# Performance work log

Hardware: AMD Instinct MI355X
Metric: run time of the kernel (lower is better)

## Reference

```python
import jax, jax.numpy as jnp
import numpy as np

N_HEADS = 32
N_KV_HEADS = 8


def _rope_tables(T, half_dim):
    # standard rotary angle tables: theta_i = 10000^(-2i/D)
    inv_freq = 1.0 / (10000.0 ** (np.arange(half_dim, dtype=np.float32) / half_dim))
    ang = np.arange(T, dtype=np.float32)[:, None] * inv_freq[None, :]  # [T, D/2]
    return jnp.asarray(np.sin(ang)), jnp.asarray(np.cos(ang))


def setup_inputs() -> dict:
    key = jax.random.key(0)
    ks = jax.random.split(key, 5)
    B, T, C = 1, 2048, 2048
    hd = C // N_HEADS  # 64
    kv_dim = N_KV_HEADS * hd  # 512
    w_scale = 0.02
    x = jax.random.normal(ks[0], (B, T, C), dtype=jnp.float32)
    Wq = jax.random.normal(ks[1], (C, C), dtype=jnp.float32) * w_scale
    Wk = jax.random.normal(ks[2], (C, kv_dim), dtype=jnp.float32) * w_scale
    Wv = jax.random.normal(ks[3], (C, kv_dim), dtype=jnp.float32) * w_scale
    Wo = jax.random.normal(ks[4], (C, C), dtype=jnp.float32) * w_scale
    rope_sin, rope_cos = _rope_tables(T, hd // 2)
    return {"x": x, "Wq": Wq, "Wk": Wk, "Wv": Wv, "Wo": Wo,
            "rope_sin": rope_sin, "rope_cos": rope_cos, "swa_window": 1024}


def apply_rope(x, sin, cos):
    # x: [B, T, H, D]; sin/cos: [T, D/2]; interleaved-pair rotation
    B, T, H, D = x.shape
    xr = x.reshape(B, T, H, D // 2, 2)
    x1, x2 = xr[..., 0], xr[..., 1]
    s = sin[None, :, None, :]
    c = cos[None, :, None, :]
    o1 = x1 * c - x2 * s
    o2 = x1 * s + x2 * c
    return jnp.stack((o1, o2), axis=-1).reshape(B, T, H, D)


def reference(x, Wq, Wk, Wv, Wo, rope_sin, rope_cos, swa_window):
    B, T, C = x.shape
    hd = C // N_HEADS
    g = N_HEADS // N_KV_HEADS
    q = (x @ Wq).reshape(B, T, N_HEADS, hd)
    k = (x @ Wk).reshape(B, T, N_KV_HEADS, hd)
    v = (x @ Wv).reshape(B, T, N_KV_HEADS, hd)
    q = apply_rope(q, rope_sin, rope_cos)
    k = apply_rope(k, rope_sin, rope_cos)
    # GQA: expand kv heads (repeat_interleave along head dim)
    k = jnp.repeat(k, g, axis=2)
    v = jnp.repeat(v, g, axis=2)
    q = q.transpose(0, 2, 1, 3)  # [B, H, T, D]
    k = k.transpose(0, 2, 1, 3)
    v = v.transpose(0, 2, 1, 3)
    scores = jnp.einsum('bhqd,bhkd->bhqk', q, k) / jnp.sqrt(jnp.float32(hd))
    idx = jnp.arange(T)
    rel = idx[:, None] - idx[None, :]  # query_pos - key_pos
    # masked-out: future tokens (rel < 0) or older than the sliding window
    masked = (rel < 0) | (rel > swa_window)
    scores = jnp.where(masked[None, None], jnp.float32(-1e30), scores)
    attn = jax.nn.softmax(scores, axis=-1)
    out = jnp.einsum('bhqk,bhkd->bhqd', attn, v)
    out = out.transpose(0, 2, 1, 3).reshape(B, T, C)
    return out @ Wo
```

## Files before the change

### kernel.cpp

```cpp
#include <hip/hip_runtime.h>

typedef __attribute__((ext_vector_type(8))) short short8;
typedef __attribute__((ext_vector_type(4))) float f32x4;
typedef unsigned short u16;

#define T_SEQ 2048
#define C_DIM 2048
#define QKV_N 3072
#define HD 64
#define QSCALE 0.18033688011112042f


static __device__ __forceinline__ u16 f2bf(float f) {
    unsigned u = __builtin_bit_cast(unsigned, f);
    unsigned rounding = 0x7fffu + ((u >> 16) & 1u);
    return (u16)((u + rounding) >> 16);
}

static __device__ __forceinline__ void gld_lds16(void* lds, const void* g) {
    __builtin_amdgcn_global_load_lds(
        (const __attribute__((address_space(1))) unsigned int*)g,
        (__attribute__((address_space(3))) unsigned int*)lds, 16, 0, 0);
}


__global__ __launch_bounds__(256) void prep_all(const float* __restrict__ x,
                                                const float* __restrict__ Wq,
                                                const float* __restrict__ Wk,
                                                const float* __restrict__ Wv,
                                                const float* __restrict__ Wo,
                                                u16* __restrict__ xb,
                                                u16* __restrict__ Wt,
                                                u16* __restrict__ Wot) {
    __shared__ float tile[32][33];
    int bx = blockIdx.x;
    if (bx >= 160) {
        int id = (bx - 160) * 64 + blockIdx.y;
        int i = (id * 256 + threadIdx.x) * 4;
        f32x4 v = *(const f32x4*)(x + i);
        u16* o = xb + i;
        o[0] = f2bf(v[0]); o[1] = f2bf(v[1]); o[2] = f2bf(v[2]); o[3] = f2bf(v[3]);
        return;
    }
    const float* W; u16* D; int N, row_off;
    if (bx < 64)      { W = Wq; D = Wt;  N = 2048; row_off = 0;    }
    else if (bx < 80) { W = Wk; D = Wt;  N = 512;  row_off = 2048; bx -= 64; }
    else if (bx < 96) { W = Wv; D = Wt;  N = 512;  row_off = 2560; bx -= 80; }
    else              { W = Wo; D = Wot; N = 2048; row_off = 0;    bx -= 96; }
    int n0 = bx * 32, k0 = blockIdx.y * 32;
    int tx = threadIdx.x & 31, ty = threadIdx.x >> 5;
#pragma unroll
    for (int i = 0; i < 4; i++)
        tile[ty + i * 8][tx] = W[(size_t)(k0 + ty + i * 8) * N + n0 + tx];
    __syncthreads();
#pragma unroll
    for (int i = 0; i < 4; i++)
        D[(size_t)(row_off + n0 + ty + i * 8) * 2048 + k0 + tx] = f2bf(tile[tx][ty + i * 8]);
}


__global__ __launch_bounds__(256) void gemm_qkv(const u16* __restrict__ A,
                                                const u16* __restrict__ BT,
                                                const float* __restrict__ sn,
                                                const float* __restrict__ cs,
                                                u16* __restrict__ qb,
                                                u16* __restrict__ kb,
                                                u16* __restrict__ vb) {
    const int K = 2048;
    __shared__ alignas(16) u16 As[2][128][64];
    __shared__ alignas(16) u16 Bs[2][96][64];
    const int m0 = blockIdx.x * 128;
    const int bn0 = blockIdx.y * 96;
    const int w = threadIdx.x >> 6, lane = threadIdx.x & 63;
    const int lo = lane & 15, hi = lane >> 4;
    const int wr = w >> 1, wc = w & 1;
    const int srcsw = ((lane & 7) ^ (lane >> 3)) * 8;

    f32x4 zero4 = {0.f, 0.f, 0.f, 0.f};
    f32x4 acc[4][3];
#pragma unroll
    for (int m = 0; m < 4; m++)
#pragma unroll
        for (int n = 0; n < 3; n++) acc[m][n] = zero4;

    auto stage = [&](int buf, int k0) {
#pragma unroll
        for (int j = 0; j < 7; j++) {
            int s = j * 4 + w;
            if (s < 16) {
                int row = s * 8 + (lane >> 3);
                gld_lds16((char*)&As[buf][0][0] + s * 1024,
                          A + (size_t)(m0 + row) * K + k0 + srcsw);
            } else {
                int s2 = s - 16;
                int row = s2 * 8 + (lane >> 3);
                gld_lds16((char*)&Bs[buf][0][0] + s2 * 1024,
                          BT + (size_t)(bn0 + row) * K + k0 + srcsw);
            }
        }
    };

    stage(0, 0);
    __syncthreads();
    const int nk = K >> 6;
    for (int t = 0; t < nk; t++) {
        const int cur = t & 1;
        if (t + 1 < nk) stage(cur ^ 1, (t + 1) * 64);
#pragma unroll
        for (int kk = 0; kk < 2; kk++) {
            const int csw = ((kk * 4 + hi) ^ (lo & 7)) << 4;
            short8 a[4], b[3];
#pragma unroll
            for (int m = 0; m < 4; m++) {
                int r = wr * 64 + m * 16 + lo;
                a[m] = *(const short8*)((const char*)&As[cur][0][0] + r * 128 + csw);
            }
#pragma unroll
            for (int n = 0; n < 3; n++) {
                int r = wc * 48 + n * 16 + lo;
                b[n] = *(const short8*)((const char*)&Bs[cur][0][0] + r * 128 + csw);
            }
#pragma unroll
            for (int m = 0; m < 4; m++)
#pragma unroll
                for (int n = 0; n < 3; n++)
                    acc[m][n] = __builtin_amdgcn_mfma_f32_16x16x32_bf16(a[m], b[n], acc[m][n], 0, 0, 0);
        }
        __syncthreads();
    }
    const bool odd = (lo & 1);
#pragma unroll
    for (int m = 0; m < 4; m++)
#pragma unroll
        for (int n = 0; n < 3; n++) {
            const int col = bn0 + wc * 48 + n * 16 + lo;
#pragma unroll
            for (int r = 0; r < 4; r++) {
                const int trow = m0 + wr * 64 + m * 16 + hi * 4 + r;
                float v = acc[m][n][r];
                float p = __shfl_xor(v, 1);
                if (col >= 2560) {
                    vb[(size_t)trow * 512 + (col - 2560)] = f2bf(v);
                } else {
                    const int pr = (col & 63) >> 1;
                    const float s = sn[trow * 32 + pr], c = cs[trow * 32 + pr];
                    float o = odd ? (p * s + v * c) : (v * c - p * s);
                    if (col < 2048) {
                        qb[(size_t)trow * C_DIM + col] = f2bf(o * QSCALE);
                    } else {
                        const int cc = col - 2048;
                        kb[((size_t)(cc >> 6) * T_SEQ + trow) * 64 + (cc & 63)] = f2bf(o);
                    }
                }
            }
        }
}


template <int NF>
__global__ __launch_bounds__(256) void gemm_bt(const u16* __restrict__ A,
                                               const u16* __restrict__ BT,
                                               float* __restrict__ C,
                                               int M, int N, int K) {
    __shared__ alignas(16) u16 As[2][128][64];
    __shared__ alignas(16) u16 Bs[2][32 * NF][64];
    const int m0 = blockIdx.x * 128;
    const int bn0 = blockIdx.y * (32 * NF);
    const int w = threadIdx.x >> 6, lane = threadIdx.x & 63;
    const int lo = lane & 15, hi = lane >> 4;
    const int wr = w >> 1, wc = w & 1;
    const int srcsw = ((lane & 7) ^ (lane >> 3)) * 8;

    f32x4 zero4 = {0.f, 0.f, 0.f, 0.f};
    f32x4 acc[4][NF];
#pragma unroll
    for (int m = 0; m < 4; m++)
#pragma unroll
        for (int n = 0; n < NF; n++) acc[m][n] = zero4;

    const int NSEG = 16 + 4 * NF;
    auto stage = [&](int buf, int k0) {
#pragma unroll
        for (int j = 0; j < NSEG / 4; j++) {
            int s = j * 4 + w;
            if (s < 16) {
                int row = s * 8 + (lane >> 3);
                gld_lds16((char*)&As[buf][0][0] + s * 1024,
                          A + (size_t)(m0 + row) * K + k0 + srcsw);
            } else {
                int s2 = s - 16;
                int row = s2 * 8 + (lane >> 3);
                gld_lds16((char*)&Bs[buf][0][0] + s2 * 1024,
                          BT + (size_t)(bn0 + row) * K + k0 + srcsw);
            }
        }
    };

    stage(0, 0);
    __syncthreads();
    const int nk = K >> 6;
    for (int t = 0; t < nk; t++) {
        const int cur = t & 1;
        if (t + 1 < nk) stage(cur ^ 1, (t + 1) * 64);
#pragma unroll
        for (int kk = 0; kk < 2; kk++) {
            const int csw = ((kk * 4 + hi) ^ (lo & 7)) << 4;
            short8 a[4], b[NF];
#pragma unroll
            for (int m = 0; m < 4; m++) {
                int r = wr * 64 + m * 16 + lo;
                a[m] = *(const short8*)((const char*)&As[cur][0][0] + r * 128 + csw);
            }
#pragma unroll
            for (int n = 0; n < NF; n++) {
                int r = wc * 16 * NF + n * 16 + lo;
                b[n] = *(const short8*)((const char*)&Bs[cur][0][0] + r * 128 + csw);
            }
#pragma unroll
            for (int m = 0; m < 4; m++)
#pragma unroll
                for (int n = 0; n < NF; n++)
                    acc[m][n] = __builtin_amdgcn_mfma_f32_16x16x32_bf16(a[m], b[n], acc[m][n], 0, 0, 0);
        }
        __syncthreads();
    }
#pragma unroll
    for (int m = 0; m < 4; m++)
#pragma unroll
        for (int n = 0; n < NF; n++) {
            int col = bn0 + wc * 16 * NF + n * 16 + lo;
#pragma unroll
            for (int r = 0; r < 4; r++) {
                int row = m0 + wr * 64 + m * 16 + hi * 4 + r;
                C[(size_t)row * N + col] = acc[m][n][r];
            }
        }
}


__global__ __launch_bounds__(256) void vtrans(const u16* __restrict__ vb,
                                              u16* __restrict__ vt) {
    __shared__ unsigned tile[64][65];
    const int kvh = blockIdx.x >> 5, t0 = (blockIdx.x & 31) * 64;
    const int tx = threadIdx.x & 63, ty = threadIdx.x >> 6;
#pragma unroll
    for (int i = 0; i < 16; i++) {
        int r = ty * 16 + i;
        tile[r][tx] = vb[(size_t)(t0 + r) * 512 + kvh * 64 + tx];
    }
    __syncthreads();
#pragma unroll
    for (int i = 0; i < 16; i++) {
        int d = ty * 16 + i;
        vt[((size_t)kvh * 64 + d) * T_SEQ + t0 + tx] = (u16)tile[tx][d];
    }
}


__global__ __launch_bounds__(256) void attn_fwd(const u16* __restrict__ qb,
                                                const u16* __restrict__ kb,
                                                const u16* __restrict__ vt,
                                                u16* __restrict__ ob,
                                                const int* __restrict__ winp) {
    __shared__ alignas(16) char KsB[2][8192];
    __shared__ alignas(16) char VsB[2][8192];
    __shared__ alignas(16) u16 Ps[4][16][64];
    const int window = *winp;
    const int h = blockIdx.y, kvh = h >> 2;
    const int q0 = blockIdx.x * 64;
    const int w = threadIdx.x >> 6, lane = threadIdx.x & 63;
    const int lo = lane & 15, hi = lane >> 4;

    const int qrow = q0 + w * 16 + lo;
    const short8 qa0 = *(const short8*)(qb + (size_t)qrow * C_DIM + h * HD + hi * 8);
    const short8 qa1 = *(const short8*)(qb + (size_t)qrow * C_DIM + h * HD + 32 + hi * 8);

    f32x4 zero4 = {0.f, 0.f, 0.f, 0.f};
    f32x4 acc[4];
#pragma unroll
    for (int dt = 0; dt < 4; dt++) acc[dt] = zero4;
    float lreg[4] = {0.f, 0.f, 0.f, 0.f};

    int kt0 = q0 - window; if (kt0 < 0) kt0 = 0; kt0 &= ~63;
    const int qlo_w = q0 + w * 16, qhi_w = qlo_w + 15;
    const int nt = (q0 + 64 - kt0) >> 6;

    auto stage = [&](int buf, int kt) {
#pragma unroll
        for (int j = 0; j < 2; j++) {
            int c = (w * 2 + j) * 64 + lane;
            int rr = c >> 3, sc = (c & 7) ^ (rr & 7);
            gld_lds16(KsB[buf] + (w * 2 + j) * 1024,
                      kb + ((size_t)kvh * T_SEQ + kt + rr) * 64 + sc * 8);
            gld_lds16(VsB[buf] + (w * 2 + j) * 1024,
                      vt + ((size_t)kvh * 64 + rr) * T_SEQ + kt + sc * 8);
        }
    };

    stage(0, kt0);
    __syncthreads();
    for (int i = 0; i < nt; i++) {
        const int kt = kt0 + i * 64;
        const int cur = i & 1;
        if (i + 1 < nt) stage(cur ^ 1, kt + 64);
        if (kt <= qhi_w && kt + 63 >= qlo_w - window) {
            const bool interior = (kt + 63 <= qlo_w) && (qhi_w - kt <= window);
            f32x4 s0, s1, s2, s3;
            __builtin_amdgcn_s_setprio(1);
            {
#define QK_TILE(SD, NT)                                                              \
                {                                                                    \
                    int key = (NT) * 16 + lo;                                        \
                    const short8 kf0 = *(const short8*)(KsB[cur] + key * 128 + ((hi ^ (key & 7)) << 4));       \
                    const short8 kf1 = *(const short8*)(KsB[cur] + key * 128 + (((4 + hi) ^ (key & 7)) << 4)); \
                    f32x4 z = zero4;                                                 \
                    z = __builtin_amdgcn_mfma_f32_16x16x32_bf16(qa0, kf0, z, 0, 0, 0);\
                    z = __builtin_amdgcn_mfma_f32_16x16x32_bf16(qa1, kf1, z, 0, 0, 0);\
                    SD = z;                                                          \
                }
                QK_TILE(s0, 0) QK_TILE(s1, 1) QK_TILE(s2, 2) QK_TILE(s3, 3)
#undef QK_TILE
            }
            __builtin_amdgcn_s_setprio(0);
            if (!interior) {
#define MASK_TILE(SD, NT)                                                            \
                {                                                                    \
                    int key = kt + (NT) * 16 + lo;                                   \
                    _Pragma("unroll")                                                \
                    for (int r = 0; r < 4; r++) {                                    \
                        int q = qlo_w + hi * 4 + r;                                  \
                        if ((unsigned)(q - key) > (unsigned)window) SD[r] = -1e30f;  \
                    }                                                                \
                }
                MASK_TILE(s0, 0) MASK_TILE(s1, 1) MASK_TILE(s2, 2) MASK_TILE(s3, 3)
#undef MASK_TILE
            }
#define EXP_TILE(SD, NT)                                                             \
            {                                                                        \
                _Pragma("unroll")                                                    \
                for (int r = 0; r < 4; r++) {                                        \
                    float p = __builtin_amdgcn_exp2f(SD[r]);                         \
                    lreg[r] += p;                                                    \
                    int q16 = hi * 4 + r;                                            \
                    Ps[w][q16][((NT) * 16 + lo) ^ ((q16 & 7) << 3)] = f2bf(p);       \
                }                                                                    \
            }
            EXP_TILE(s0, 0) EXP_TILE(s1, 1) EXP_TILE(s2, 2) EXP_TILE(s3, 3)
#undef EXP_TILE
            const short8 pa0 = *(const short8*)&Ps[w][lo][(hi ^ (lo & 7)) << 3];
            const short8 pa1 = *(const short8*)&Ps[w][lo][((4 + hi) ^ (lo & 7)) << 3];
            __builtin_amdgcn_s_setprio(1);
#pragma unroll
            for (int dt = 0; dt < 4; dt++) {
                int d = dt * 16 + lo;
                const short8 vf0 = *(const short8*)(VsB[cur] + d * 128 + ((hi ^ (d & 7)) << 4));
                const short8 vf1 = *(const short8*)(VsB[cur] + d * 128 + (((4 + hi) ^ (d & 7)) << 4));
                acc[dt] = __builtin_amdgcn_mfma_f32_16x16x32_bf16(pa0, vf0, acc[dt], 0, 0, 0);
                acc[dt] = __builtin_amdgcn_mfma_f32_16x16x32_bf16(pa1, vf1, acc[dt], 0, 0, 0);
            }
            __builtin_amdgcn_s_setprio(0);
        }
        __syncthreads();
    }
    float inv[4];
#pragma unroll
    for (int r = 0; r < 4; r++) {
        float l = lreg[r];
        l += __shfl_xor(l, 1);
        l += __shfl_xor(l, 2);
        l += __shfl_xor(l, 4);
        l += __shfl_xor(l, 8);
        inv[r] = 1.0f / l;
    }
#pragma unroll
    for (int dt = 0; dt < 4; dt++)
#pragma unroll
        for (int r = 0; r < 4; r++) {
            int q = qlo_w + hi * 4 + r;
            ob[(size_t)q * C_DIM + h * HD + dt * 16 + lo] = f2bf(acc[dt][r] * inv[r]);
        }
}


extern "C" void kernel_launch(void* const* d_in, const int* in_sizes, int n_in,
                              void* d_out, int out_size, void* d_ws, size_t ws_size,
                              hipStream_t stream) {
    const float* x  = (const float*)d_in[0];
    const float* Wq = (const float*)d_in[1];
    const float* Wk = (const float*)d_in[2];
    const float* Wv = (const float*)d_in[3];
    const float* Wo = (const float*)d_in[4];
    const float* rs = (const float*)d_in[5];
    const float* rc = (const float*)d_in[6];
    const int*  win = (const int*)d_in[7];
    float* out = (float*)d_out;

    char* w = (char*)d_ws;
    u16*   xb   = (u16*)(w);
    u16*   Wt   = (u16*)(w + (8ull  << 20));
    u16*   Wot  = (u16*)(w + (20ull << 20));
    u16*   qb   = (u16*)(w + (28ull << 20));
    u16*   kbuf = (u16*)(w + (36ull << 20));
    u16*   vb   = (u16*)(w + (38ull << 20));
    u16*   vtb  = (u16*)(w + (40ull << 20));
    u16*   attb = (u16*)(w + (42ull << 20));

    prep_all<<<dim3(224, 64), 256, 0, stream>>>(x, Wq, Wk, Wv, Wo, xb, Wt, Wot);
    gemm_qkv<<<dim3(16, 32), 256, 0, stream>>>(xb, Wt, rs, rc, qb, kbuf, vb);
    vtrans<<<256, 256, 0, stream>>>(vb, vtb);
    attn_fwd<<<dim3(32, 32), 256, 0, stream>>>(qb, kbuf, vtb, attb, win);
    gemm_bt<2><<<dim3(16, 32), 256, 0, stream>>>(attb, Wot, out, 2048, 2048, 2048);
}
```

Baseline: 228.9 us.

## Read K/V directly from global in attention and shrink QKV GEMM N-tile

The attention kernel stops staging K and V tiles into double-buffered LDS with block-wide barriers. Each wave now loads its MFMA fragments straight from global memory and iterates only over the key tiles its own 16 queries need. Separately, the QKV GEMM N-tile shrinks from 96 to 64 columns, giving more blocks (16x48) with fewer accumulators each. This removes the LDS staging and sync overhead but adds redundant global/L2 traffic, since all four waves re-read the same K/V rows.

```diff
diff --git a/kernel.cpp b/kernel.cpp
--- a/kernel.cpp
+++ b/kernel.cpp
@@ -68,24 +68,24 @@
                                                 u16* __restrict__ vb) {
     const int K = 2048;
     __shared__ alignas(16) u16 As[2][128][64];
-    __shared__ alignas(16) u16 Bs[2][96][64];
+    __shared__ alignas(16) u16 Bs[2][64][64];
     const int m0 = blockIdx.x * 128;
-    const int bn0 = blockIdx.y * 96;
+    const int bn0 = blockIdx.y * 64;
     const int w = threadIdx.x >> 6, lane = threadIdx.x & 63;
     const int lo = lane & 15, hi = lane >> 4;
     const int wr = w >> 1, wc = w & 1;
     const int srcsw = ((lane & 7) ^ (lane >> 3)) * 8;
 
     f32x4 zero4 = {0.f, 0.f, 0.f, 0.f};
-    f32x4 acc[4][3];
+    f32x4 acc[4][2];
 #pragma unroll
     for (int m = 0; m < 4; m++)
 #pragma unroll
-        for (int n = 0; n < 3; n++) acc[m][n] = zero4;
+        for (int n = 0; n < 2; n++) acc[m][n] = zero4;
 
     auto stage = [&](int buf, int k0) {
 #pragma unroll
-        for (int j = 0; j < 7; j++) {
+        for (int j = 0; j < 6; j++) {
             int s = j * 4 + w;
             if (s < 16) {
                 int row = s * 8 + (lane >> 3);
@@ -109,21 +109,21 @@
 #pragma unroll
         for (int kk = 0; kk < 2; kk++) {
             const int csw = ((kk * 4 + hi) ^ (lo & 7)) << 4;
-            short8 a[4], b[3];
+            short8 a[4], b[2];
 #pragma unroll
             for (int m = 0; m < 4; m++) {
                 int r = wr * 64 + m * 16 + lo;
                 a[m] = *(const short8*)((const char*)&As[cur][0][0] + r * 128 + csw);
             }
 #pragma unroll
-            for (int n = 0; n < 3; n++) {
-                int r = wc * 48 + n * 16 + lo;
+            for (int n = 0; n < 2; n++) {
+                int r = wc * 32 + n * 16 + lo;
                 b[n] = *(const short8*)((const char*)&Bs[cur][0][0] + r * 128 + csw);
             }
 #pragma unroll
             for (int m = 0; m < 4; m++)
 #pragma unroll
-                for (int n = 0; n < 3; n++)
+                for (int n = 0; n < 2; n++)
                     acc[m][n] = __builtin_amdgcn_mfma_f32_16x16x32_bf16(a[m], b[n], acc[m][n], 0, 0, 0);
         }
         __syncthreads();
@@ -132,8 +132,8 @@
 #pragma unroll
     for (int m = 0; m < 4; m++)
 #pragma unroll
-        for (int n = 0; n < 3; n++) {
-            const int col = bn0 + wc * 48 + n * 16 + lo;
+        for (int n = 0; n < 2; n++) {
+            const int col = bn0 + wc * 32 + n * 16 + lo;
 #pragma unroll
             for (int r = 0; r < 4; r++) {
                 const int trow = m0 + wr * 64 + m * 16 + hi * 4 + r;
@@ -262,8 +262,6 @@
                                                 const u16* __restrict__ vt,
                                                 u16* __restrict__ ob,
                                                 const int* __restrict__ winp) {
-    __shared__ alignas(16) char KsB[2][8192];
-    __shared__ alignas(16) char VsB[2][8192];
     __shared__ alignas(16) u16 Ps[4][16][64];
     const int window = *winp;
     const int h = blockIdx.y, kvh = h >> 2;
@@ -271,96 +269,78 @@
     const int w = threadIdx.x >> 6, lane = threadIdx.x & 63;
     const int lo = lane & 15, hi = lane >> 4;
 
-    const int qrow = q0 + w * 16 + lo;
+    const int qlo_w = q0 + w * 16, qhi_w = qlo_w + 15;
+    const int qrow = qlo_w + lo;
     const short8 qa0 = *(const short8*)(qb + (size_t)qrow * C_DIM + h * HD + hi * 8);
     const short8 qa1 = *(const short8*)(qb + (size_t)qrow * C_DIM + h * HD + 32 + hi * 8);
 
+    const u16* kbase = kb + (size_t)kvh * T_SEQ * HD;
+    const u16* vbase = vt + (size_t)kvh * HD * T_SEQ;
+
     f32x4 zero4 = {0.f, 0.f, 0.f, 0.f};
     f32x4 acc[4];
 #pragma unroll
     for (int dt = 0; dt < 4; dt++) acc[dt] = zero4;
     float lreg[4] = {0.f, 0.f, 0.f, 0.f};
 
-    int kt0 = q0 - window; if (kt0 < 0) kt0 = 0; kt0 &= ~63;
-    const int qlo_w = q0 + w * 16, qhi_w = qlo_w + 15;
-    const int nt = (q0 + 64 - kt0) >> 6;
-
-    auto stage = [&](int buf, int kt) {
-#pragma unroll
-        for (int j = 0; j < 2; j++) {
-            int c = (w * 2 + j) * 64 + lane;
-            int rr = c >> 3, sc = (c & 7) ^ (rr & 7);
-            gld_lds16(KsB[buf] + (w * 2 + j) * 1024,
-                      kb + ((size_t)kvh * T_SEQ + kt + rr) * 64 + sc * 8);
-            gld_lds16(VsB[buf] + (w * 2 + j) * 1024,
-                      vt + ((size_t)kvh * 64 + rr) * T_SEQ + kt + sc * 8);
-        }
-    };
-
-    stage(0, kt0);
-    __syncthreads();
-    for (int i = 0; i < nt; i++) {
-        const int kt = kt0 + i * 64;
-        const int cur = i & 1;
-        if (i + 1 < nt) stage(cur ^ 1, kt + 64);
-        if (kt <= qhi_w && kt + 63 >= qlo_w - window) {
-            const bool interior = (kt + 63 <= qlo_w) && (qhi_w - kt <= window);
-            f32x4 s0, s1, s2, s3;
-            __builtin_amdgcn_s_setprio(1);
-            {
+    int ktb = qlo_w - window; if (ktb < 0) ktb = 0; ktb &= ~63;
+
+    for (int kt = ktb; kt <= qhi_w; kt += 64) {
+        const bool interior = (kt + 63 <= qlo_w) && (qhi_w - kt <= window);
+        f32x4 s0, s1, s2, s3;
+        __builtin_amdgcn_s_setprio(1);
+        {
 #define QK_TILE(SD, NT)                                                              \
-                {                                                                    \
-                    int key = (NT) * 16 + lo;                                        \
-                    const short8 kf0 = *(const short8*)(KsB[cur] + key * 128 + ((hi ^ (key & 7)) << 4));       \
-                    const short8 kf1 = *(const short8*)(KsB[cur] + key * 128 + (((4 + hi) ^ (key & 7)) << 4)); \
-                    f32x4 z = zero4;                                                 \
-                    z = __builtin_amdgcn_mfma_f32_16x16x32_bf16(qa0, kf0, z, 0, 0, 0);\
-                    z = __builtin_amdgcn_mfma_f32_16x16x32_bf16(qa1, kf1, z, 0, 0, 0);\
-                    SD = z;                                                          \
-                }
-                QK_TILE(s0, 0) QK_TILE(s1, 1) QK_TILE(s2, 2) QK_TILE(s3, 3)
+            {                                                                        \
+                const u16* kp = kbase + (size_t)(kt + (NT) * 16 + lo) * HD + hi * 8; \
+                const short8 kf0 = *(const short8*)(kp);                             \
+                const short8 kf1 = *(const short8*)(kp + 32);                        \
+                f32x4 z = zero4;                                                     \
+                z = __builtin_amdgcn_mfma_f32_16x16x32_bf16(qa0, kf0, z, 0, 0, 0);   \
+                z = __builtin_amdgcn_mfma_f32_16x16x32_bf16(qa1, kf1, z, 0, 0, 0);   \
+                SD = z;                                                              \
+            }
+            QK_TILE(s0, 0) QK_TILE(s1, 1) QK_TILE(s2, 2) QK_TILE(s3, 3)
 #undef QK_TILE
-            }
-            __builtin_amdgcn_s_setprio(0);
-            if (!interior) {
+        }
+        __builtin_amdgcn_s_setprio(0);
+        if (!interior) {
 #define MASK_TILE(SD, NT)                                                            \
-                {                                                                    \
-                    int key = kt + (NT) * 16 + lo;                                   \
-                    _Pragma("unroll")                                                \
-                    for (int r = 0; r < 4; r++) {                                    \
-                        int q = qlo_w + hi * 4 + r;                                  \
-                        if ((unsigned)(q - key) > (unsigned)window) SD[r] = -1e30f;  \
-                    }                                                                \
-                }
-                MASK_TILE(s0, 0) MASK_TILE(s1, 1) MASK_TILE(s2, 2) MASK_TILE(s3, 3)
-#undef MASK_TILE
-            }
-#define EXP_TILE(SD, NT)                                                             \
             {                                                                        \
+                int key = kt + (NT) * 16 + lo;                                       \
                 _Pragma("unroll")                                                    \
                 for (int r = 0; r < 4; r++) {                                        \
-                    float p = __builtin_amdgcn_exp2f(SD[r]);                         \
-                    lreg[r] += p;                                                    \
-                    int q16 = hi * 4 + r;                                            \
-                    Ps[w][q16][((NT) * 16 + lo) ^ ((q16 & 7) << 3)] = f2bf(p);       \
+                    int q = qlo_w + hi * 4 + r;                                      \
+                    if ((unsigned)(q - key) > (unsigned)window) SD[r] = -1e30f;      \
                 }                                                                    \
             }
-            EXP_TILE(s0, 0) EXP_TILE(s1, 1) EXP_TILE(s2, 2) EXP_TILE(s3, 3)
+            MASK_TILE(s0, 0) MASK_TILE(s1, 1) MASK_TILE(s2, 2) MASK_TILE(s3, 3)
+#undef MASK_TILE
+        }
+#define EXP_TILE(SD, NT)                                                             \
+        {                                                                            \
+            _Pragma("unroll")                                                        \
+            for (int r = 0; r < 4; r++) {                                            \
+                float p = __builtin_amdgcn_exp2f(SD[r]);                             \
+                lreg[r] += p;                                                        \
+                int q16 = hi * 4 + r;                                                \
+                Ps[w][q16][((NT) * 16 + lo) ^ ((q16 & 7) << 3)] = f2bf(p);           \
+            }                                                                        \
+        }
+        EXP_TILE(s0, 0) EXP_TILE(s1, 1) EXP_TILE(s2, 2) EXP_TILE(s3, 3)
 #undef EXP_TILE
-            const short8 pa0 = *(const short8*)&Ps[w][lo][(hi ^ (lo & 7)) << 3];
-            const short8 pa1 = *(const short8*)&Ps[w][lo][((4 + hi) ^ (lo & 7)) << 3];
-            __builtin_amdgcn_s_setprio(1);
-#pragma unroll
-            for (int dt = 0; dt < 4; dt++) {
-                int d = dt * 16 + lo;
-                const short8 vf0 = *(const short8*)(VsB[cur] + d * 128 + ((hi ^ (d & 7)) << 4));
-                const short8 vf1 = *(const short8*)(VsB[cur] + d * 128 + (((4 + hi) ^ (d & 7)) << 4));
-                acc[dt] = __builtin_amdgcn_mfma_f32_16x16x32_bf16(pa0, vf0, acc[dt], 0, 0, 0);
-                acc[dt] = __builtin_amdgcn_mfma_f32_16x16x32_bf16(pa1, vf1, acc[dt], 0, 0, 0);
-            }
-            __builtin_amdgcn_s_setprio(0);
-        }
-        __syncthreads();
+        const short8 pa0 = *(const short8*)&Ps[w][lo][(hi ^ (lo & 7)) << 3];
+        const short8 pa1 = *(const short8*)&Ps[w][lo][((4 + hi) ^ (lo & 7)) << 3];
+        __builtin_amdgcn_s_setprio(1);
+#pragma unroll
+        for (int dt = 0; dt < 4; dt++) {
+            const u16* vp = vbase + (size_t)(dt * 16 + lo) * T_SEQ + kt + hi * 8;
+            const short8 vf0 = *(const short8*)(vp);
+            const short8 vf1 = *(const short8*)(vp + 32);
+            acc[dt] = __builtin_amdgcn_mfma_f32_16x16x32_bf16(pa0, vf0, acc[dt], 0, 0, 0);
+            acc[dt] = __builtin_amdgcn_mfma_f32_16x16x32_bf16(pa1, vf1, acc[dt], 0, 0, 0);
+        }
+        __builtin_amdgcn_s_setprio(0);
     }
     float inv[4];
 #pragma unroll
@@ -406,7 +386,7 @@
     u16*   attb = (u16*)(w + (42ull << 20));
 
     prep_all<<<dim3(224, 64), 256, 0, stream>>>(x, Wq, Wk, Wv, Wo, xb, Wt, Wot);
-    gemm_qkv<<<dim3(16, 32), 256, 0, stream>>>(xb, Wt, rs, rc, qb, kbuf, vb);
+    gemm_qkv<<<dim3(16, 48), 256, 0, stream>>>(xb, Wt, rs, rc, qb, kbuf, vb);
     vtrans<<<256, 256, 0, stream>>>(vb, vtb);
     attn_fwd<<<dim3(32, 32), 256, 0, stream>>>(qb, kbuf, vtb, attb, win);
     gemm_bt<2><<<dim3(16, 32), 256, 0, stream>>>(attb, Wot, out, 2048, 2048, 2048);
```

After: 306.6 us. +33.9%, slower.
